# Optimization experiments

Hardware: AMD Instinct MI355X
Metric: run time of the kernel (lower is better)

The kernel has to match this reference:

```python
import jax, jax.numpy as jnp
import numpy as np

J = 21        # joints per skeleton
DIM = 3       # cfg.dataset.dim
NH = 7        # node_hsize = 2*DIM + 1
H = 4         # cfg.model.gat_heads
HD = 64       # h_dim
ALPHA = 0.2   # cfg.model.gat_alpha (LeakyReLU slope)


def setup_inputs() -> dict:
    key = jax.random.key(0)
    k1, k2, k3, k4, k5 = jax.random.split(key, 5)
    inputs = jax.random.normal(k1, (16, 1024, J * NH), dtype=jnp.float32)
    starts = jnp.arange(8, dtype=jnp.int64) * 128
    seq_start_end = jnp.stack([starts, starts + 128], axis=1)  # [8,2], unused in forward
    # Xavier-ish scaled params
    W_heads = jax.random.normal(k2, (H, NH, HD), dtype=jnp.float32) * (1.414 / np.sqrt(NH + HD) * np.sqrt(6) / 1.732)
    a_heads = jax.random.normal(k3, (H, 2 * HD), dtype=jnp.float32) * 0.1
    W_out = jax.random.normal(k4, (H * HD, HD), dtype=jnp.float32) * 0.08
    a_out = jax.random.normal(k5, (2 * HD,), dtype=jnp.float32) * 0.1
    return {"inputs": inputs, "seq_start_end": seq_start_end,
            "W_heads": W_heads, "a_heads": a_heads,
            "W_out": W_out, "a_out": a_out}


def _gat_attend(h, a1, a2):
    # h: [..., J, D]; a1,a2: [..., D] broadcastable; FC graph -> no adj mask
    f1 = jnp.sum(h * a1[..., None, :], axis=-1)          # [..., J]
    f2 = jnp.sum(h * a2[..., None, :], axis=-1)          # [..., J]
    e = jax.nn.leaky_relu(f1[..., :, None] + f2[..., None, :], ALPHA)  # [..., J, J]
    attn = jax.nn.softmax(e, axis=-1)
    return jnp.matmul(attn, h)                           # [..., J, D]


def reference(inputs, seq_start_end, W_heads, a_heads, W_out, a_out):
    F_, P, _ = inputs.shape
    # rebuild per-node graph features: [offset(dim) | loc(dim) | S(1)] per joint
    off = inputs[..., : J * DIM].reshape(F_, P, J, DIM)
    loc = inputs[..., J * DIM: 2 * J * DIM].reshape(F_, P, J, DIM)
    S = inputs[..., 2 * J * DIM:].reshape(F_, P, J, 1)
    x = jnp.concatenate([off, loc, S], axis=-1)          # [F,P,J,NH]
    # multi-head GAT layer (concat=True -> elu)
    h = jnp.einsum('fpjn,hnd->fphjd', x, W_heads)        # [F,P,H,J,HD]
    a1 = a_heads[:, :HD]                                 # [H,HD]
    a2 = a_heads[:, HD:]
    hp = jax.nn.elu(_gat_attend(h, a1[None, None], a2[None, None]))  # [F,P,H,J,HD]
    xcat = jnp.transpose(hp, (0, 1, 3, 2, 4)).reshape(F_, P, J, H * HD)
    # output GAT layer (concat=False -> raw h_prime), then outer elu + log_softmax
    h2 = jnp.einsum('fpjn,nd->fpjd', xcat, W_out)        # [F,P,J,HD]
    hp2 = _gat_attend(h2, a_out[None, None, :HD], a_out[None, None, HD:])
    out = jax.nn.log_softmax(jax.nn.elu(hp2), axis=-1)   # log_softmax over feature dim
    return out.reshape(F_, P, J * HD)
```

## Files before the change

### kernel.cpp

```cpp
#include <hip/hip_runtime.h>
#include <hip/hip_bf16.h>
#include <math.h>

#define J   21
#define NH  7
#define H   4
#define HD  64
#define ALPHA 0.2f

#define HPS  264
#define JPA  40
#define JPT  24
#define JA2  32
#define F12S 24
#define A2S  24

#define ROW2 68
#define LDS_FLOATS 7932

typedef __attribute__((ext_vector_type(8))) short short8;
typedef __attribute__((ext_vector_type(4))) float floatx4;

static __device__ __forceinline__ short f2bf(float f) {
    __hip_bfloat16 h = __float2bfloat16(f);
    return __builtin_bit_cast(short, h);
}
static __device__ __forceinline__ short hi16(float f) {
    return (short)(__builtin_bit_cast(unsigned, f) >> 16);
}
static __device__ __forceinline__ unsigned pack2hi(float lo, float hi) {
    return __builtin_amdgcn_perm(__builtin_bit_cast(unsigned, hi),
                                 __builtin_bit_cast(unsigned, lo), 0x07060302u);
}
static __device__ __forceinline__ float elu(float a) {
    return (a > 0.f) ? a : (__expf(a) - 1.f);
}

__global__ void preconv(const float* __restrict__ Wo, const float* __restrict__ Wh,
                        const float* __restrict__ ah, short* __restrict__ ws) {
    int t = blockIdx.x * 256 + threadIdx.x;
    if (t < 16384) {
        int n = t >> 8, k = t & 255;
        ws[t] = f2bf(Wo[k * HD + n]);
    } else if (t < 18432) {
        int i = t - 16384;
        int hh = i >> 9, d = (i >> 3) & 63, n = i & 7;
        ws[t] = (n < 7) ? f2bf(Wh[(hh * NH + n) * HD + d]) : (short)0;
    } else if (t < 18496) {
        int i = t - 18432;
        int hh = i >> 4, s = (i >> 3) & 1, n = i & 7;
        float acc = 0.f;
        if (n < 7) {
            for (int d = 0; d < HD; d++)
                acc += Wh[(hh * NH + n) * HD + d] * ah[hh * 2 * HD + s * HD + d];
        }
        ((float*)(ws + 18432))[i] = acc;
    }
}

__global__ __launch_bounds__(256, 4)
void gat_kernel(const float* __restrict__ inp,
                const float* __restrict__ ao,
                const short* __restrict__ ws,
                float* __restrict__ out)
{
    __shared__ __align__(16) float smem[LDS_FLOATS];
    short* hp_bf    = (short*)smem;
    float* xs_raw   = smem + 2904;
    float* f1o      = smem;
    float* f2o      = smem + 24;
    short* attn2_bf = (short*)smem + 96;
    short* attn_bf  = (short*)(smem + 2904);
    float* f1       = smem + 4664;
    float* f2       = smem + 4760;
    short* h_t      = (short*)(smem + 4856);
    float* h2       = smem + 4856;
    short* h2_t     = (short*)(smem + 6300);

    const short* WoT  = ws;
    const short* WhT  = ws + 16384;
    const float* whaF = (const float*)(ws + 18432);

    const int t    = threadIdx.x;
    const int w    = t >> 6;
    const int lane = t & 63;
    const int quad = lane >> 4;
    const int col  = lane & 15;
    const int rc   = (16 + col < 21) ? (16 + col) : 21;

    const size_t pair = blockIdx.x;
    const float* ip = inp + pair * (size_t)(J * NH);

    for (int e = t; e < 440; e += 256) smem[2904 + e] = 0.f;
    if (t < 4) smem[7928 + t] = 0.f;
    __syncthreads();
    if (t < J * NH) {
        float v = ip[t];
        int j, k;
        if (t < 63)       { j = t / 3;        k = t % 3; }
        else if (t < 126) { j = (t - 63) / 3; k = 3 + (t - 63) % 3; }
        else              { j = t - 126;      k = 6; }
        ((short*)(smem + 2904))[j * JPA + k] = hi16(v);
        smem[0 + t] = v;
    }
    __syncthreads();

    {
        const short* x_bf = (const short*)(smem + 2904);
        short8 xa0 = *(const short8*)(x_bf + col * JPA + quad * 8);
        short8 xa1 = *(const short8*)(x_bf + rc  * JPA + quad * 8);
        floatx4 c0[4], c1[4];
        #pragma unroll
        for (int nt = 0; nt < 4; nt++) { c0[nt] = (floatx4){0,0,0,0}; c1[nt] = (floatx4){0,0,0,0}; }
        #pragma unroll
        for (int nt = 0; nt < 4; nt++) {
            short8 b = *(const short8*)(WhT + ((w * 64 + nt * 16 + col) << 3) + quad * 8);
            c0[nt] = __builtin_amdgcn_mfma_f32_16x16x32_bf16(xa0, b, c0[nt], 0, 0, 0);
            c1[nt] = __builtin_amdgcn_mfma_f32_16x16x32_bf16(xa1, b, c1[nt], 0, 0, 0);
        }
        #pragma unroll
        for (int nt = 0; nt < 4; nt++) {
            short* colbase = h_t + (w * 64 + nt * 16 + col) * JPT;
            #pragma unroll
            for (int r = 0; r < 4; r++) {
                colbase[quad * 4 + r] = hi16(c0[nt][r]);
                int row1 = 16 + quad * 4 + r;
                if (row1 < J) colbase[row1] = hi16(c1[nt][r]);
                else if (row1 < JPT) colbase[row1] = 0;
            }
        }
        if (t < 84) {
            int hh = t / 21, j = t - hh * 21;
            const float* xr = smem;
            float x0 = xr[j*3+0], x1 = xr[j*3+1], x2 = xr[j*3+2];
            float x3 = xr[63+j*3+0], x4 = xr[63+j*3+1], x5 = xr[63+j*3+2];
            float x6 = xr[126+j];
            const float* wp = whaF + hh * 16;
            f1[hh * F12S + j] = x0*wp[0] + x1*wp[1] + x2*wp[2] + x3*wp[3]
                              + x4*wp[4] + x5*wp[5] + x6*wp[6];
            f2[hh * F12S + j] = x0*wp[8] + x1*wp[9] + x2*wp[10] + x3*wp[11]
                              + x4*wp[12] + x5*wp[13] + x6*wp[14];
        }
    }
    __syncthreads();

    if (t < H * 22) {
        int hh = t / 22, i = t % 22;
        unsigned* rowp = (unsigned*)(attn_bf + (hh * 22 + i) * JPA);
        if (i < J) {
            float fi = f1[hh * F12S + i];
            const float* f2r = f2 + hh * F12S;
            float ev[J];
            float m = -1e30f;
            #pragma unroll
            for (int c4 = 0; c4 < 5; c4++) {
                float4 fv = ((const float4*)f2r)[c4];
                float e;
                e = fi + fv.x; e = (e >= 0.f) ? e : ALPHA * e; ev[c4*4+0] = e; m = fmaxf(m, e);
                e = fi + fv.y; e = (e >= 0.f) ? e : ALPHA * e; ev[c4*4+1] = e; m = fmaxf(m, e);
                e = fi + fv.z; e = (e >= 0.f) ? e : ALPHA * e; ev[c4*4+2] = e; m = fmaxf(m, e);
                e = fi + fv.w; e = (e >= 0.f) ? e : ALPHA * e; ev[c4*4+3] = e; m = fmaxf(m, e);
            }
            { float e = fi + f2r[20]; e = (e >= 0.f) ? e : ALPHA * e; ev[20] = e; m = fmaxf(m, e); }
            float ssum = 0.f;
            #pragma unroll
            for (int j = 0; j < J; j++) { float ex = __expf(ev[j] - m); ev[j] = ex; ssum += ex; }
            float inv = 1.f / ssum;
            #pragma unroll
            for (int k = 0; k < 10; k++)
                rowp[k] = pack2hi(ev[2*k] * inv, ev[2*k+1] * inv);
            rowp[10] = pack2hi(ev[20] * inv, 0.f);
            #pragma unroll
            for (int k = 11; k < 16; k++) rowp[k] = 0;
        } else {
            #pragma unroll
            for (int k = 0; k < 16; k++) rowp[k] = 0;
        }
    }
    __syncthreads();

    {
        short8 aa0 = *(const short8*)(attn_bf + (w * 22 + col) * JPA + quad * 8);
        short8 aa1 = *(const short8*)(attn_bf + (w * 22 + rc)  * JPA + quad * 8);
        floatx4 c0[4], c1[4];
        #pragma unroll
        for (int nt = 0; nt < 4; nt++) { c0[nt] = (floatx4){0,0,0,0}; c1[nt] = (floatx4){0,0,0,0}; }
        #pragma unroll
        for (int nt = 0; nt < 4; nt++) {
            short8 b = *(const short8*)(h_t + (w * 64 + nt * 16 + col) * JPT + quad * 8);
            c0[nt] = __builtin_amdgcn_mfma_f32_16x16x32_bf16(aa0, b, c0[nt], 0, 0, 0);
            c1[nt] = __builtin_amdgcn_mfma_f32_16x16x32_bf16(aa1, b, c1[nt], 0, 0, 0);
        }
        #pragma unroll
        for (int nt = 0; nt < 4; nt++) {
            #pragma unroll
            for (int r = 0; r < 4; r++) {
                int row0 = quad * 4 + r;
                hp_bf[row0 * HPS + w * 64 + nt * 16 + col] = hi16(elu(c0[nt][r]));
                int row1 = 16 + quad * 4 + r;
                if (row1 < J)
                    hp_bf[row1 * HPS + w * 64 + nt * 16 + col] = hi16(elu(c1[nt][r]));
                else if (row1 == 21)
                    hp_bf[21 * HPS + w * 64 + nt * 16 + col] = 0;
            }
        }
    }
    __syncthreads();

    {
        floatx4 d0 = {0,0,0,0}, d1 = {0,0,0,0};
        #pragma unroll
        for (int s = 0; s < 8; s++) {
            short8 a0 = *(const short8*)(hp_bf + col * HPS + s * 32 + quad * 8);
            short8 a1 = *(const short8*)(hp_bf + rc  * HPS + s * 32 + quad * 8);
            short8 b  = *(const short8*)(WoT + (w * 16 + col) * 256 + s * 32 + quad * 8);
            d0 = __builtin_amdgcn_mfma_f32_16x16x32_bf16(a0, b, d0, 0, 0, 0);
            d1 = __builtin_amdgcn_mfma_f32_16x16x32_bf16(a1, b, d1, 0, 0, 0);
        }
        const int c = w * 16 + col;
        #pragma unroll
        for (int r = 0; r < 4; r++) {
            h2[(quad * 4 + r) * ROW2 + c] = d0[r];
            int row1 = 16 + quad * 4 + r;
            if (row1 < J) h2[row1 * ROW2 + c] = d1[r];
        }
        short* cb = h2_t + c * JPT;
        *(uint2*)(cb + quad * 4) = make_uint2(pack2hi(d0[0], d0[1]), pack2hi(d0[2], d0[3]));
        if (quad == 0)
            *(uint2*)(cb + 16) = make_uint2(pack2hi(d1[0], d1[1]), pack2hi(d1[2], d1[3]));
        else if (quad == 1)
            *(uint2*)(cb + 20) = make_uint2(pack2hi(d1[0], 0.f), 0u);
    }
    __syncthreads();

    if (t < 2 * J) {
        int which = t / J, j = t % J;
        const float4* hrow = (const float4*)(h2 + j * ROW2);
        const float4* ap   = (const float4*)(ao + which * HD);
        float sacc = 0.f;
        #pragma unroll
        for (int k = 0; k < HD / 4; k++) {
            float4 hv = hrow[k], av = ap[k];
            sacc += hv.x*av.x + hv.y*av.y + hv.z*av.z + hv.w*av.w;
        }
        if (which == 0) f1o[j] = sacc; else f2o[j] = sacc;
    }
    __syncthreads();

    if (t < 22) {
        unsigned* rowp = (unsigned*)(attn2_bf + t * JA2);
        if (t < J) {
            float fi = f1o[t];
            float ev[J];
            float m = -1e30f;
            #pragma unroll
            for (int c4 = 0; c4 < 5; c4++) {
                float4 fv = ((const float4*)f2o)[c4];
                float e;
                e = fi + fv.x; e = (e >= 0.f) ? e : ALPHA * e; ev[c4*4+0] = e; m = fmaxf(m, e);
                e = fi + fv.y; e = (e >= 0.f) ? e : ALPHA * e; ev[c4*4+1] = e; m = fmaxf(m, e);
                e = fi + fv.z; e = (e >= 0.f) ? e : ALPHA * e; ev[c4*4+2] = e; m = fmaxf(m, e);
                e = fi + fv.w; e = (e >= 0.f) ? e : ALPHA * e; ev[c4*4+3] = e; m = fmaxf(m, e);
            }
            { float e = fi + f2o[20]; e = (e >= 0.f) ? e : ALPHA * e; ev[20] = e; m = fmaxf(m, e); }
            float ssum = 0.f;
            #pragma unroll
            for (int j = 0; j < J; j++) { float ex = __expf(ev[j] - m); ev[j] = ex; ssum += ex; }
            float inv = 1.f / ssum;
            #pragma unroll
            for (int k = 0; k < 10; k++)
                rowp[k] = pack2hi(ev[2*k] * inv, ev[2*k+1] * inv);
            rowp[10] = pack2hi(ev[20] * inv, 0.f);
            #pragma unroll
            for (int k = 11; k < 16; k++) rowp[k] = 0;
        } else {
            #pragma unroll
            for (int k = 0; k < 16; k++) rowp[k] = 0;
        }
    }
    __syncthreads();

    {
        const int mt = w & 1;
        const int rh = w >> 1;
        const int arow = mt * 16 + col;
        const int ar = (arow < 21) ? arow : 21;
        short8 a = *(const short8*)(attn2_bf + ar * JA2 + quad * 8);
        floatx4 acc[4];
        #pragma unroll
        for (int nt = 0; nt < 4; nt++) {
            short8 b = *(const short8*)(h2_t + (nt * 16 + col) * JPT + quad * 8);
            floatx4 z = {0,0,0,0};
            acc[nt] = __builtin_amdgcn_mfma_f32_16x16x32_bf16(a, b, z, 0, 0, 0);
        }
        float* outp = out + pair * (size_t)(J * HD);
        #pragma unroll
        for (int rr = 0; rr < 2; rr++) {
            int r = rh * 2 + rr;
            int row = mt * 16 + quad * 4 + r;
            float v0 = elu(acc[0][r]), v1 = elu(acc[1][r]);
            float v2 = elu(acc[2][r]), v3 = elu(acc[3][r]);
            float s = __expf(v0) + __expf(v1) + __expf(v2) + __expf(v3);
            s += __shfl_xor(s, 1);
            s += __shfl_xor(s, 2);
            s += __shfl_xor(s, 4);
            s += __shfl_xor(s, 8);
            float ls = __logf(s);
            if (row < J) {
                outp[row * HD +      col] = v0 - ls;
                outp[row * HD + 16 + col] = v1 - ls;
                outp[row * HD + 32 + col] = v2 - ls;
                outp[row * HD + 48 + col] = v3 - ls;
            }
        }
    }
}

extern "C" void kernel_launch(void* const* d_in, const int* in_sizes, int n_in,
                              void* d_out, int out_size, void* d_ws, size_t ws_size,
                              hipStream_t stream) {
    const float* inp = (const float*)d_in[0];
    const float* Wh  = (const float*)d_in[2];
    const float* ah  = (const float*)d_in[3];
    const float* Wo  = (const float*)d_in[4];
    const float* ao  = (const float*)d_in[5];
    float* outp = (float*)d_out;
    short* ws   = (short*)d_ws;

    hipLaunchKernelGGL(preconv, dim3(73), dim3(256), 0, stream, Wo, Wh, ah, ws);

    const int pairs = in_sizes[0] / (J * NH);
    hipLaunchKernelGGL(gat_kernel, dim3(pairs), dim3(256), 0, stream,
                       inp, ao, (const short*)ws, outp);
}
```

Before: 225.2 us.

## Fold output attention vector into W_out and pack MFMA result stores

Precomputes W_out·a_out in bf16 during preconv, so the output-layer f1/f2 scores come from an MFMA over hp on wave 0. This removes the fp32 h2 staging buffer, one block barrier and the scalar dot-product stage. The first-layer MFMA outputs and the attention·h products are now written as packed 64-bit bf16 stores, and the second product swaps operands to make the stores contiguous. The f1/f2 scores now come from bf16-rounded hp and bf16 folded weights instead of fp32 h2, which slightly changes numerics.

Result: slower. 234.5 us (+4.1%).

```diff
diff --git a/kernel.cpp b/kernel.cpp
--- a/kernel.cpp
+++ b/kernel.cpp
@@ -11,11 +11,8 @@
 #define HPS  264
 #define JPA  40
 #define JPT  24
-#define JA2  32
 #define F12S 24
-#define A2S  24
-
-#define ROW2 68
+
 #define LDS_FLOATS 7932
 
 typedef __attribute__((ext_vector_type(8))) short short8;
@@ -37,7 +34,8 @@
 }
 
 __global__ void preconv(const float* __restrict__ Wo, const float* __restrict__ Wh,
-                        const float* __restrict__ ah, short* __restrict__ ws) {
+                        const float* __restrict__ ah, const float* __restrict__ ao,
+                        short* __restrict__ ws) {
     int t = blockIdx.x * 256 + threadIdx.x;
     if (t < 16384) {
         int n = t >> 8, k = t & 255;
@@ -55,31 +53,40 @@
                 acc += Wh[(hh * NH + n) * HD + d] * ah[hh * 2 * HD + s * HD + d];
         }
         ((float*)(ws + 18432))[i] = acc;
+    } else if (t < 22592) {
+        int i = t - 18496;
+        int s = i >> 8, k = i & 255;
+        short v = 0;
+        if (s < 2) {
+            float acc = 0.f;
+            for (int d = 0; d < HD; d++)
+                acc += Wo[k * HD + d] * ao[s * HD + d];
+            v = f2bf(acc);
+        }
+        ws[18560 + i] = v;
     }
 }
 
 __global__ __launch_bounds__(256, 4)
 void gat_kernel(const float* __restrict__ inp,
-                const float* __restrict__ ao,
                 const short* __restrict__ ws,
                 float* __restrict__ out)
 {
     __shared__ __align__(16) float smem[LDS_FLOATS];
     short* hp_bf    = (short*)smem;
-    float* xs_raw   = smem + 2904;
-    float* f1o      = smem;
-    float* f2o      = smem + 24;
     short* attn2_bf = (short*)smem + 96;
     short* attn_bf  = (short*)(smem + 2904);
     float* f1       = smem + 4664;
     float* f2       = smem + 4760;
+    float* f1o      = smem + 4664;
+    float* f2o      = smem + 4688;
     short* h_t      = (short*)(smem + 4856);
-    float* h2       = smem + 4856;
     short* h2_t     = (short*)(smem + 6300);
 
     const short* WoT  = ws;
     const short* WhT  = ws + 16384;
     const float* whaF = (const float*)(ws + 18432);
+    const short* WoaT = ws + 18560;
 
     const int t    = threadIdx.x;
     const int w    = t >> 6;
@@ -101,7 +108,7 @@
         else if (t < 126) { j = (t - 63) / 3; k = 3 + (t - 63) % 3; }
         else              { j = t - 126;      k = 6; }
         ((short*)(smem + 2904))[j * JPA + k] = hi16(v);
-        smem[0 + t] = v;
+        smem[t] = v;
     }
     __syncthreads();
 
@@ -109,25 +116,20 @@
         const short* x_bf = (const short*)(smem + 2904);
         short8 xa0 = *(const short8*)(x_bf + col * JPA + quad * 8);
         short8 xa1 = *(const short8*)(x_bf + rc  * JPA + quad * 8);
-        floatx4 c0[4], c1[4];
-        #pragma unroll
-        for (int nt = 0; nt < 4; nt++) { c0[nt] = (floatx4){0,0,0,0}; c1[nt] = (floatx4){0,0,0,0}; }
         #pragma unroll
         for (int nt = 0; nt < 4; nt++) {
             short8 b = *(const short8*)(WhT + ((w * 64 + nt * 16 + col) << 3) + quad * 8);
-            c0[nt] = __builtin_amdgcn_mfma_f32_16x16x32_bf16(xa0, b, c0[nt], 0, 0, 0);
-            c1[nt] = __builtin_amdgcn_mfma_f32_16x16x32_bf16(xa1, b, c1[nt], 0, 0, 0);
-        }
-        #pragma unroll
-        for (int nt = 0; nt < 4; nt++) {
-            short* colbase = h_t + (w * 64 + nt * 16 + col) * JPT;
-            #pragma unroll
-            for (int r = 0; r < 4; r++) {
-                colbase[quad * 4 + r] = hi16(c0[nt][r]);
-                int row1 = 16 + quad * 4 + r;
-                if (row1 < J) colbase[row1] = hi16(c1[nt][r]);
-                else if (row1 < JPT) colbase[row1] = 0;
-            }
+            floatx4 z = {0.f, 0.f, 0.f, 0.f};
+            floatx4 c0 = __builtin_amdgcn_mfma_f32_16x16x32_bf16(xa0, b, z, 0, 0, 0);
+            floatx4 c1 = __builtin_amdgcn_mfma_f32_16x16x32_bf16(xa1, b, z, 0, 0, 0);
+            short* cb = h_t + (w * 64 + nt * 16 + col) * JPT;
+            *(uint2*)(cb + quad * 4) =
+                make_uint2(pack2hi(c0[0], c0[1]), pack2hi(c0[2], c0[3]));
+            if (quad == 0)
+                *(uint2*)(cb + 16) =
+                    make_uint2(pack2hi(c1[0], c1[1]), pack2hi(c1[2], c1[3]));
+            else if (quad == 1)
+                *(uint2*)(cb + 20) = make_uint2(pack2hi(c1[0], 0.f), 0u);
         }
         if (t < 84) {
             int hh = t / 21, j = t - hh * 21;
@@ -180,28 +182,23 @@
     __syncthreads();
 
     {
-        short8 aa0 = *(const short8*)(attn_bf + (w * 22 + col) * JPA + quad * 8);
-        short8 aa1 = *(const short8*)(attn_bf + (w * 22 + rc)  * JPA + quad * 8);
-        floatx4 c0[4], c1[4];
-        #pragma unroll
-        for (int nt = 0; nt < 4; nt++) { c0[nt] = (floatx4){0,0,0,0}; c1[nt] = (floatx4){0,0,0,0}; }
-        #pragma unroll
-        for (int nt = 0; nt < 4; nt++) {
-            short8 b = *(const short8*)(h_t + (w * 64 + nt * 16 + col) * JPT + quad * 8);
-            c0[nt] = __builtin_amdgcn_mfma_f32_16x16x32_bf16(aa0, b, c0[nt], 0, 0, 0);
-            c1[nt] = __builtin_amdgcn_mfma_f32_16x16x32_bf16(aa1, b, c1[nt], 0, 0, 0);
-        }
-        #pragma unroll
-        for (int nt = 0; nt < 4; nt++) {
-            #pragma unroll
-            for (int r = 0; r < 4; r++) {
-                int row0 = quad * 4 + r;
-                hp_bf[row0 * HPS + w * 64 + nt * 16 + col] = hi16(elu(c0[nt][r]));
-                int row1 = 16 + quad * 4 + r;
-                if (row1 < J)
-                    hp_bf[row1 * HPS + w * 64 + nt * 16 + col] = hi16(elu(c1[nt][r]));
-                else if (row1 == 21)
-                    hp_bf[21 * HPS + w * 64 + nt * 16 + col] = 0;
+        short8 bb0 = *(const short8*)(attn_bf + (w * 22 + col) * JPA + quad * 8);
+        const int am  = 16 + col;
+        const int amc = (am < 21) ? am : 21;
+        short8 bb1 = *(const short8*)(attn_bf + (w * 22 + amc) * JPA + quad * 8);
+        #pragma unroll
+        for (int dt = 0; dt < 4; dt++) {
+            short8 a = *(const short8*)(h_t + (w * 64 + dt * 16 + col) * JPT + quad * 8);
+            floatx4 z = {0.f, 0.f, 0.f, 0.f};
+            floatx4 c0 = __builtin_amdgcn_mfma_f32_16x16x32_bf16(a, bb0, z, 0, 0, 0);
+            floatx4 c1 = __builtin_amdgcn_mfma_f32_16x16x32_bf16(a, bb1, z, 0, 0, 0);
+            *(uint2*)(hp_bf + col * HPS + w * 64 + dt * 16 + quad * 4) =
+                make_uint2(pack2hi(elu(c0[0]), elu(c0[1])),
+                           pack2hi(elu(c0[2]), elu(c0[3])));
+            if (am <= 21) {
+                *(uint2*)(hp_bf + am * HPS + w * 64 + dt * 16 + quad * 4) =
+                    make_uint2(pack2hi(elu(c1[0]), elu(c1[1])),
+                               pack2hi(elu(c1[2]), elu(c1[3])));
             }
         }
     }
@@ -218,37 +215,38 @@
             d1 = __builtin_amdgcn_mfma_f32_16x16x32_bf16(a1, b, d1, 0, 0, 0);
         }
         const int c = w * 16 + col;
-        #pragma unroll
-        for (int r = 0; r < 4; r++) {
-            h2[(quad * 4 + r) * ROW2 + c] = d0[r];
-            int row1 = 16 + quad * 4 + r;
-            if (row1 < J) h2[row1 * ROW2 + c] = d1[r];
-        }
         short* cb = h2_t + c * JPT;
         *(uint2*)(cb + quad * 4) = make_uint2(pack2hi(d0[0], d0[1]), pack2hi(d0[2], d0[3]));
         if (quad == 0)
             *(uint2*)(cb + 16) = make_uint2(pack2hi(d1[0], d1[1]), pack2hi(d1[2], d1[3]));
         else if (quad == 1)
             *(uint2*)(cb + 20) = make_uint2(pack2hi(d1[0], 0.f), 0u);
-    }
-    __syncthreads();
-
-    if (t < 2 * J) {
-        int which = t / J, j = t % J;
-        const float4* hrow = (const float4*)(h2 + j * ROW2);
-        const float4* ap   = (const float4*)(ao + which * HD);
-        float sacc = 0.f;
-        #pragma unroll
-        for (int k = 0; k < HD / 4; k++) {
-            float4 hv = hrow[k], av = ap[k];
-            sacc += hv.x*av.x + hv.y*av.y + hv.z*av.z + hv.w*av.w;
-        }
-        if (which == 0) f1o[j] = sacc; else f2o[j] = sacc;
+
+        if (w == 0) {
+            floatx4 g0 = {0,0,0,0}, g1 = {0,0,0,0};
+            #pragma unroll
+            for (int s = 0; s < 8; s++) {
+                short8 a0 = *(const short8*)(hp_bf + col * HPS + s * 32 + quad * 8);
+                short8 a1 = *(const short8*)(hp_bf + rc  * HPS + s * 32 + quad * 8);
+                short8 bg = *(const short8*)(WoaT + col * 256 + s * 32 + quad * 8);
+                g0 = __builtin_amdgcn_mfma_f32_16x16x32_bf16(a0, bg, g0, 0, 0, 0);
+                g1 = __builtin_amdgcn_mfma_f32_16x16x32_bf16(a1, bg, g1, 0, 0, 0);
+            }
+            if (col < 2) {
+                float* fo = col ? f2o : f1o;
+                #pragma unroll
+                for (int r = 0; r < 4; r++) {
+                    fo[quad * 4 + r] = g0[r];
+                    int row1 = 16 + quad * 4 + r;
+                    if (row1 < J) fo[row1] = g1[r];
+                }
+            }
+        }
     }
     __syncthreads();
 
     if (t < 22) {
-        unsigned* rowp = (unsigned*)(attn2_bf + t * JA2);
+        unsigned* rowp = (unsigned*)(attn2_bf + t * 32);
         if (t < J) {
             float fi = f1o[t];
             float ev[J];
@@ -285,7 +283,7 @@
         const int rh = w >> 1;
         const int arow = mt * 16 + col;
         const int ar = (arow < 21) ? arow : 21;
-        short8 a = *(const short8*)(attn2_bf + ar * JA2 + quad * 8);
+        short8 a = *(const short8*)(attn2_bf + ar * 32 + quad * 8);
         floatx4 acc[4];
         #pragma unroll
         for (int nt = 0; nt < 4; nt++) {
@@ -327,9 +325,9 @@
     float* outp = (float*)d_out;
     short* ws   = (short*)d_ws;
 
-    hipLaunchKernelGGL(preconv, dim3(73), dim3(256), 0, stream, Wo, Wh, ah, ws);
+    hipLaunchKernelGGL(preconv, dim3(89), dim3(256), 0, stream, Wo, Wh, ah, ao, ws);
 
     const int pairs = in_sizes[0] / (J * NH);
     hipLaunchKernelGGL(gat_kernel, dim3(pairs), dim3(256), 0, stream,
-                       inp, ao, (const short*)ws, outp);
-}
+                       inp, (const short*)ws, outp);
+}
```

## Compute GAT softmax in registers directly as MFMA A-operand fragments

Applied to the files above, without the earlier changes.

Both attention softmax stages now run inside the MFMA matmul warps, instead of in separate thread subsets that write bf16 attention rows to shared memory. Each lane builds its own 8-element slice of the A-fragment, and the row sums are reduced with cross-quad shuffles. This removes two barriers and the LDS write and read of the attention matrices, at the cost of extra exp work in every lane. The max subtraction is dropped from the softmax, which risks overflow for large logits. The MFMA loops are also restructured to store each result right after it is computed.

New measurement: 230.2 us. +2.2%, slower.

```diff
diff --git a/kernel.cpp b/kernel.cpp
--- a/kernel.cpp
+++ b/kernel.cpp
@@ -11,11 +11,9 @@
 #define HPS  264
 #define JPA  40
 #define JPT  24
-#define JA2  32
 #define F12S 24
-#define A2S  24
-
 #define ROW2 68
+
 #define LDS_FLOATS 7932
 
 typedef __attribute__((ext_vector_type(8))) short short8;
@@ -65,17 +63,14 @@
                 float* __restrict__ out)
 {
     __shared__ __align__(16) float smem[LDS_FLOATS];
-    short* hp_bf    = (short*)smem;
-    float* xs_raw   = smem + 2904;
-    float* f1o      = smem;
-    float* f2o      = smem + 24;
-    short* attn2_bf = (short*)smem + 96;
-    short* attn_bf  = (short*)(smem + 2904);
-    float* f1       = smem + 4664;
-    float* f2       = smem + 4760;
-    short* h_t      = (short*)(smem + 4856);
-    float* h2       = smem + 4856;
-    short* h2_t     = (short*)(smem + 6300);
+    short* hp_bf  = (short*)smem;
+    float* f1o    = smem;
+    float* f2o    = smem + 24;
+    float* f1     = smem + 4664;
+    float* f2     = smem + 4760;
+    short* h_t    = (short*)(smem + 4856);
+    float* h2     = smem + 4856;
+    short* h2_t   = (short*)(smem + 6300);
 
     const short* WoT  = ws;
     const short* WhT  = ws + 16384;
@@ -101,7 +96,7 @@
         else if (t < 126) { j = (t - 63) / 3; k = 3 + (t - 63) % 3; }
         else              { j = t - 126;      k = 6; }
         ((short*)(smem + 2904))[j * JPA + k] = hi16(v);
-        smem[0 + t] = v;
+        smem[t] = v;
     }
     __syncthreads();
 
@@ -109,23 +104,18 @@
         const short* x_bf = (const short*)(smem + 2904);
         short8 xa0 = *(const short8*)(x_bf + col * JPA + quad * 8);
         short8 xa1 = *(const short8*)(x_bf + rc  * JPA + quad * 8);
-        floatx4 c0[4], c1[4];
-        #pragma unroll
-        for (int nt = 0; nt < 4; nt++) { c0[nt] = (floatx4){0,0,0,0}; c1[nt] = (floatx4){0,0,0,0}; }
         #pragma unroll
         for (int nt = 0; nt < 4; nt++) {
             short8 b = *(const short8*)(WhT + ((w * 64 + nt * 16 + col) << 3) + quad * 8);
-            c0[nt] = __builtin_amdgcn_mfma_f32_16x16x32_bf16(xa0, b, c0[nt], 0, 0, 0);
-            c1[nt] = __builtin_amdgcn_mfma_f32_16x16x32_bf16(xa1, b, c1[nt], 0, 0, 0);
-        }
-        #pragma unroll
-        for (int nt = 0; nt < 4; nt++) {
+            floatx4 z = {0.f, 0.f, 0.f, 0.f};
+            floatx4 c0 = __builtin_amdgcn_mfma_f32_16x16x32_bf16(xa0, b, z, 0, 0, 0);
+            floatx4 c1 = __builtin_amdgcn_mfma_f32_16x16x32_bf16(xa1, b, z, 0, 0, 0);
             short* colbase = h_t + (w * 64 + nt * 16 + col) * JPT;
             #pragma unroll
             for (int r = 0; r < 4; r++) {
-                colbase[quad * 4 + r] = hi16(c0[nt][r]);
+                colbase[quad * 4 + r] = hi16(c0[r]);
                 int row1 = 16 + quad * 4 + r;
-                if (row1 < J) colbase[row1] = hi16(c1[nt][r]);
+                if (row1 < J) colbase[row1] = hi16(c1[r]);
                 else if (row1 < JPT) colbase[row1] = 0;
             }
         }
@@ -144,62 +134,48 @@
     }
     __syncthreads();
 
-    if (t < H * 22) {
-        int hh = t / 22, i = t % 22;
-        unsigned* rowp = (unsigned*)(attn_bf + (hh * 22 + i) * JPA);
-        if (i < J) {
-            float fi = f1[hh * F12S + i];
-            const float* f2r = f2 + hh * F12S;
-            float ev[J];
-            float m = -1e30f;
-            #pragma unroll
-            for (int c4 = 0; c4 < 5; c4++) {
-                float4 fv = ((const float4*)f2r)[c4];
-                float e;
-                e = fi + fv.x; e = (e >= 0.f) ? e : ALPHA * e; ev[c4*4+0] = e; m = fmaxf(m, e);
-                e = fi + fv.y; e = (e >= 0.f) ? e : ALPHA * e; ev[c4*4+1] = e; m = fmaxf(m, e);
-                e = fi + fv.z; e = (e >= 0.f) ? e : ALPHA * e; ev[c4*4+2] = e; m = fmaxf(m, e);
-                e = fi + fv.w; e = (e >= 0.f) ? e : ALPHA * e; ev[c4*4+3] = e; m = fmaxf(m, e);
-            }
-            { float e = fi + f2r[20]; e = (e >= 0.f) ? e : ALPHA * e; ev[20] = e; m = fmaxf(m, e); }
-            float ssum = 0.f;
-            #pragma unroll
-            for (int j = 0; j < J; j++) { float ex = __expf(ev[j] - m); ev[j] = ex; ssum += ex; }
-            float inv = 1.f / ssum;
-            #pragma unroll
-            for (int k = 0; k < 10; k++)
-                rowp[k] = pack2hi(ev[2*k] * inv, ev[2*k+1] * inv);
-            rowp[10] = pack2hi(ev[20] * inv, 0.f);
-            #pragma unroll
-            for (int k = 11; k < 16; k++) rowp[k] = 0;
-        } else {
-            #pragma unroll
-            for (int k = 0; k < 16; k++) rowp[k] = 0;
-        }
-    }
-    __syncthreads();
-
-    {
-        short8 aa0 = *(const short8*)(attn_bf + (w * 22 + col) * JPA + quad * 8);
-        short8 aa1 = *(const short8*)(attn_bf + (w * 22 + rc)  * JPA + quad * 8);
-        floatx4 c0[4], c1[4];
-        #pragma unroll
-        for (int nt = 0; nt < 4; nt++) { c0[nt] = (floatx4){0,0,0,0}; c1[nt] = (floatx4){0,0,0,0}; }
+    {
+        float4 fqa = *(const float4*)(f2 + w * F12S + quad * 8);
+        float4 fqb = *(const float4*)(f2 + w * F12S + quad * 8 + 4);
+        float fq[8] = {fqa.x, fqa.y, fqa.z, fqa.w, fqb.x, fqb.y, fqb.z, fqb.w};
+        float fi0 = f1[w * F12S + col];
+        const int am  = 16 + col;
+        const int amc = (am < 21) ? am : 20;
+        float fi1 = f1[w * F12S + amc];
+        float e0[8], e1[8];
+        float s0 = 0.f, s1 = 0.f;
+        #pragma unroll
+        for (int j = 0; j < 8; j++) {
+            bool valid = (quad * 8 + j) < 21;
+            float a0 = fi0 + fq[j]; a0 = (a0 >= 0.f) ? a0 : ALPHA * a0;
+            float a1 = fi1 + fq[j]; a1 = (a1 >= 0.f) ? a1 : ALPHA * a1;
+            float x0 = __expf(a0); x0 = valid ? x0 : 0.f;
+            float x1 = __expf(a1); x1 = valid ? x1 : 0.f;
+            e0[j] = x0; e1[j] = x1; s0 += x0; s1 += x1;
+        }
+        s0 += __shfl_xor(s0, 16); s0 += __shfl_xor(s0, 32);
+        s1 += __shfl_xor(s1, 16); s1 += __shfl_xor(s1, 32);
+        float inv0 = 1.f / s0, inv1 = 1.f / s1;
+        short8 aa0, aa1;
+        #pragma unroll
+        for (int j = 0; j < 8; j++) {
+            aa0[j] = hi16(e0[j] * inv0);
+            aa1[j] = hi16(e1[j] * inv1);
+        }
+
         #pragma unroll
         for (int nt = 0; nt < 4; nt++) {
             short8 b = *(const short8*)(h_t + (w * 64 + nt * 16 + col) * JPT + quad * 8);
-            c0[nt] = __builtin_amdgcn_mfma_f32_16x16x32_bf16(aa0, b, c0[nt], 0, 0, 0);
-            c1[nt] = __builtin_amdgcn_mfma_f32_16x16x32_bf16(aa1, b, c1[nt], 0, 0, 0);
-        }
-        #pragma unroll
-        for (int nt = 0; nt < 4; nt++) {
+            floatx4 z = {0.f, 0.f, 0.f, 0.f};
+            floatx4 c0 = __builtin_amdgcn_mfma_f32_16x16x32_bf16(aa0, b, z, 0, 0, 0);
+            floatx4 c1 = __builtin_amdgcn_mfma_f32_16x16x32_bf16(aa1, b, z, 0, 0, 0);
             #pragma unroll
             for (int r = 0; r < 4; r++) {
                 int row0 = quad * 4 + r;
-                hp_bf[row0 * HPS + w * 64 + nt * 16 + col] = hi16(elu(c0[nt][r]));
+                hp_bf[row0 * HPS + w * 64 + nt * 16 + col] = hi16(elu(c0[r]));
                 int row1 = 16 + quad * 4 + r;
                 if (row1 < J)
-                    hp_bf[row1 * HPS + w * 64 + nt * 16 + col] = hi16(elu(c1[nt][r]));
+                    hp_bf[row1 * HPS + w * 64 + nt * 16 + col] = hi16(elu(c1[r]));
                 else if (row1 == 21)
                     hp_bf[21 * HPS + w * 64 + nt * 16 + col] = 0;
             }
@@ -247,45 +223,31 @@
     }
     __syncthreads();
 
-    if (t < 22) {
-        unsigned* rowp = (unsigned*)(attn2_bf + t * JA2);
-        if (t < J) {
-            float fi = f1o[t];
-            float ev[J];
-            float m = -1e30f;
-            #pragma unroll
-            for (int c4 = 0; c4 < 5; c4++) {
-                float4 fv = ((const float4*)f2o)[c4];
-                float e;
-                e = fi + fv.x; e = (e >= 0.f) ? e : ALPHA * e; ev[c4*4+0] = e; m = fmaxf(m, e);
-                e = fi + fv.y; e = (e >= 0.f) ? e : ALPHA * e; ev[c4*4+1] = e; m = fmaxf(m, e);
-                e = fi + fv.z; e = (e >= 0.f) ? e : ALPHA * e; ev[c4*4+2] = e; m = fmaxf(m, e);
-                e = fi + fv.w; e = (e >= 0.f) ? e : ALPHA * e; ev[c4*4+3] = e; m = fmaxf(m, e);
-            }
-            { float e = fi + f2o[20]; e = (e >= 0.f) ? e : ALPHA * e; ev[20] = e; m = fmaxf(m, e); }
-            float ssum = 0.f;
-            #pragma unroll
-            for (int j = 0; j < J; j++) { float ex = __expf(ev[j] - m); ev[j] = ex; ssum += ex; }
-            float inv = 1.f / ssum;
-            #pragma unroll
-            for (int k = 0; k < 10; k++)
-                rowp[k] = pack2hi(ev[2*k] * inv, ev[2*k+1] * inv);
-            rowp[10] = pack2hi(ev[20] * inv, 0.f);
-            #pragma unroll
-            for (int k = 11; k < 16; k++) rowp[k] = 0;
-        } else {
-            #pragma unroll
-            for (int k = 0; k < 16; k++) rowp[k] = 0;
-        }
-    }
-    __syncthreads();
-
     {
         const int mt = w & 1;
         const int rh = w >> 1;
         const int arow = mt * 16 + col;
-        const int ar = (arow < 21) ? arow : 21;
-        short8 a = *(const short8*)(attn2_bf + ar * JA2 + quad * 8);
+        const int ar = (arow < 21) ? arow : 20;
+
+        float4 fqa = *(const float4*)(f2o + quad * 8);
+        float4 fqb = *(const float4*)(f2o + quad * 8 + 4);
+        float fq[8] = {fqa.x, fqa.y, fqa.z, fqa.w, fqb.x, fqb.y, fqb.z, fqb.w};
+        float fi = f1o[ar];
+        float ev[8];
+        float ssum = 0.f;
+        #pragma unroll
+        for (int j = 0; j < 8; j++) {
+            bool valid = (quad * 8 + j) < 21;
+            float e = fi + fq[j]; e = (e >= 0.f) ? e : ALPHA * e;
+            float x = __expf(e); x = valid ? x : 0.f;
+            ev[j] = x; ssum += x;
+        }
+        ssum += __shfl_xor(ssum, 16); ssum += __shfl_xor(ssum, 32);
+        float inv = 1.f / ssum;
+        short8 a;
+        #pragma unroll
+        for (int j = 0; j < 8; j++) a[j] = hi16(ev[j] * inv);
+
         floatx4 acc[4];
         #pragma unroll
         for (int nt = 0; nt < 4; nt++) {
```
